# Kernel optimization log

Measured on AMD Instinct MI355X. Metric: run time of the kernel, lower is better.

Reference implementation:

```python
import jax, jax.numpy as jnp
import numpy as np
import math

B, C, T = 4, 512, 2048
LN_EPS = 1e-5

def setup_inputs() -> dict:
    key = jax.random.key(0)
    ks = jax.random.split(key, 12)
    s = 1.0 / math.sqrt(C)
    inp = {
        'feat': jax.random.normal(ks[0], (B, C, T), dtype=jnp.float32),
        'Wq': jax.random.normal(ks[1], (C, C), dtype=jnp.float32) * s,
        'bq': jax.random.normal(ks[2], (C,), dtype=jnp.float32) * s,
        'Wk': jax.random.normal(ks[3], (C, C), dtype=jnp.float32) * s,
        'bk': jax.random.normal(ks[4], (C,), dtype=jnp.float32) * s,
        'Wv': jax.random.normal(ks[5], (C, C), dtype=jnp.float32) * s,
        'bv': jax.random.normal(ks[6], (C,), dtype=jnp.float32) * s,
        'Ws': jax.random.normal(ks[7], (C, C), dtype=jnp.float32) * s,
        'bs': jax.random.normal(ks[8], (C,), dtype=jnp.float32) * s,
        'Wl': jax.random.normal(ks[9], (C,), dtype=jnp.float32) * s,
        'bl': jax.random.normal(ks[10], (1,), dtype=jnp.float32) * s,
    }
    return inp

def reference(feat, Wq, bq, Wk, bk, Wv, bv, Ws, bs, Wl, bl):
    d = feat.shape[1]
    # 1x1 Conv1d == per-position linear over channels. feat: [B,C,T]
    value = jnp.einsum('oc,bct->bto', Wv, feat) + bv          # [B,T,C]
    query = jnp.einsum('oc,bct->bto', Wq, feat) + bq          # [B,T,C]
    key_  = jnp.einsum('oc,bct->bct', Wk, feat) + bk[:, None] # [B,C,T]
    f = jnp.einsum('btc,bcs->bts', query, key_) / math.sqrt(d)
    f = jax.nn.softmax(f, axis=2)                             # [B,T,T]
    y = jnp.einsum('bts,bsc->btc', f, value)                  # [B,T,C]
    f_score = jax.nn.sigmoid(jnp.einsum('btc,c->bt', y, Wl) + bl[0])
    z = jnp.einsum('bts,bsc->btc', 1.0 - f, value)            # [B,T,C]
    b_score = 1.0 - jax.nn.sigmoid(jnp.einsum('btc,c->bt', z, Wl) + bl[0])
    f_score = (f_score + b_score) / 2.0
    y_ct = jnp.einsum('oc,btc->bot', Ws, y) + bs[:, None]     # smooth conv, [B,C,T]
    out = feat + y_ct
    # LayerNorm over (C, T) jointly, default affine (weight=1, bias=0)
    mu = jnp.mean(out, axis=(1, 2), keepdims=True)
    var = jnp.mean(jnp.square(out - mu), axis=(1, 2), keepdims=True)
    out = (out - mu) * jax.lax.rsqrt(var + LN_EPS)
    return out, f_score
```

## Files before the change

kernel.cpp:

```cpp
#include <hip/hip_runtime.h>
#include <hip/hip_bf16.h>

#define BB 4
#define CC 512
#define TT 2048
static constexpr long CT  = (long)CC * TT;
static constexpr long TC  = (long)TT * CC;
static constexpr long TTT = (long)TT * TT;
static constexpr float SM_SCALE = 0.04419417382415922f;

typedef __bf16 bf16;
typedef __attribute__((ext_vector_type(8))) __bf16 bf16x8;
typedef __attribute__((ext_vector_type(4))) __bf16 bf16x4;
typedef __attribute__((ext_vector_type(4))) float f32x4;

__device__ __forceinline__ void load_lds16(const bf16* g, bf16* l)
{
    __builtin_amdgcn_global_load_lds(
        (const __attribute__((address_space(1))) void*)g,
        (__attribute__((address_space(3))) void*)l, 16, 0, 0);
}

#define FENCE asm volatile("" ::: "memory")

template <int TM, int TN, int WR, int WC, int BK>
struct CorePipe {
    static constexpr int THREADS = WR * WC * 64;
    static constexpr int MI = TM / (WR * 16);
    static constexpr int NI = TN / (WC * 16);
    static constexpr int CPR = BK / 8;
    static constexpr int RSH = (BK == 64) ? 3 : 2;
    static constexpr int CMASK = CPR - 1;
    static constexpr int CHUNKS = (TM + TN) * CPR;
    static constexpr int ACH = TM * CPR;
    static constexpr int CPT = CHUNKS / THREADS;
    static_assert(CPT * THREADS == CHUNKS, "chunk divisibility");
    static_assert(CPT == 4, "vmcnt literals below assume 4 loads/thread/tile");

    __device__ static __forceinline__ void stage(
        const bf16* __restrict__ Ab, const bf16* __restrict__ Bb,
        int K, int m0, int n0, int t, int p, bf16* As, bf16* Bs, int tid)
    {
#pragma unroll
        for (int i = 0; i < CPT; ++i) {
            int c = tid + i * THREADS;
            if (c < ACH) {
                int row = c >> RSH;
                int gc  = (c & CMASK) ^ (row & CMASK);
                load_lds16(Ab + (long)(m0 + row) * K + t * BK + gc * 8,
                           As + p * (TM * BK) + c * 8);
            } else {
                int d = c - ACH;
                int row = d >> RSH;
                int gc  = (d & CMASK) ^ (row & CMASK);
                load_lds16(Bb + (long)(n0 + row) * K + t * BK + gc * 8,
                           Bs + p * (TN * BK) + d * 8);
            }
        }
    }

    __device__ static __forceinline__ void run(
        const bf16* __restrict__ Ab, const bf16* __restrict__ Bb,
        int K, int m0, int n0, bf16* As, bf16* Bs, f32x4 (&acc)[MI][NI])
    {
        const int tid  = threadIdx.x;
        const int lane = tid & 63;
        const int wid  = tid >> 6;
        const int wr = (wid / WC) * (MI * 16);
        const int wc = (wid % WC) * (NI * 16);
        const int lm = lane & 15;
        const int lq = lane >> 4;
        const int nt = K / BK;

        stage(Ab, Bb, K, m0, n0, 0, 0, As, Bs, tid);
        stage(Ab, Bb, K, m0, n0, 1, 1, As, Bs, tid);
        asm volatile("s_waitcnt vmcnt(4)" ::: "memory");
        FENCE; __builtin_amdgcn_s_barrier(); FENCE;

        for (int t = 0; t < nt; ++t) {
            const int p = t & 1;
            const bf16* Ap = As + p * (TM * BK);
            const bf16* Bp = Bs + p * (TN * BK);
            bf16x8 af[BK / 32][MI], bfr[BK / 32][NI];
#pragma unroll
            for (int ks = 0; ks < BK / 32; ++ks) {
#pragma unroll
                for (int i = 0; i < MI; ++i) {
                    int ar = wr + i * 16 + lm;
                    int cc = (ks * 4 + lq) ^ (ar & CMASK);
                    af[ks][i] = *(const bf16x8*)(Ap + ar * BK + cc * 8);
                }
#pragma unroll
                for (int i = 0; i < NI; ++i) {
                    int br = wc + i * 16 + lm;
                    int cc = (ks * 4 + lq) ^ (br & CMASK);
                    bfr[ks][i] = *(const bf16x8*)(Bp + br * BK + cc * 8);
                }
            }
            asm volatile("s_waitcnt lgkmcnt(0)" ::: "memory");
            __builtin_amdgcn_sched_barrier(0);
            FENCE; __builtin_amdgcn_s_barrier(); FENCE;
            if (t + 2 < nt)
                stage(Ab, Bb, K, m0, n0, t + 2, p, As, Bs, tid);
            __builtin_amdgcn_s_setprio(1);
#pragma unroll
            for (int ks = 0; ks < BK / 32; ++ks)
#pragma unroll
                for (int mi = 0; mi < MI; ++mi)
#pragma unroll
                    for (int ni = 0; ni < NI; ++ni)
                        acc[mi][ni] = __builtin_amdgcn_mfma_f32_16x16x32_bf16(
                            af[ks][mi], bfr[ks][ni], acc[mi][ni], 0, 0, 0);
            __builtin_amdgcn_s_setprio(0);
            if (t + 1 < nt) {
                if (t + 2 < nt)
                    asm volatile("s_waitcnt vmcnt(4)" ::: "memory");
                else
                    asm volatile("s_waitcnt vmcnt(0)" ::: "memory");
                FENCE; __builtin_amdgcn_s_barrier(); FENCE;
            }
        }
    }
};

using CP = CorePipe<128, 128, 4, 2, 64>;

struct CoreQVPipe {
    static constexpr int THREADS = 512;
    static constexpr int MI = 2;
    static constexpr int NI = 4;
    static constexpr int BK = 64;
    static constexpr int CPR = 8, RSH = 3, CMASK = 7;
    static constexpr int ACH = 128 * 8;
    static constexpr int CHUNKS = 256 * 8;
    static constexpr int CPT = CHUNKS / THREADS;

    __device__ static __forceinline__ void stage(
        const bf16* __restrict__ Ab, const bf16* __restrict__ Bq,
        const bf16* __restrict__ Bv, int m0, int t, int p,
        bf16* As, bf16* Bs, int tid)
    {
#pragma unroll
        for (int i = 0; i < CPT; ++i) {
            int c = tid + i * THREADS;
            if (c < ACH) {
                int row = c >> RSH;
                int gc  = (c & CMASK) ^ (row & CMASK);
                load_lds16(Ab + (long)(m0 + row) * 512 + t * 64 + gc * 8,
                           As + p * (128 * 64) + c * 8);
            } else {
                int d = c - ACH;
                int row = d >> RSH;
                int gc  = (d & CMASK) ^ (row & CMASK);
                const bf16* src = (row < 64)
                    ? Bq + (long)row * 512
                    : Bv + (long)(row - 64) * 512;
                load_lds16(src + t * 64 + gc * 8, Bs + p * (128 * 64) + d * 8);
            }
        }
    }

    __device__ static __forceinline__ void run(
        const bf16* __restrict__ Ab, const bf16* __restrict__ Bq,
        const bf16* __restrict__ Bv,
        int m0, bf16* As, bf16* Bs, f32x4 (&acc)[MI][NI])
    {
        const int tid  = threadIdx.x;
        const int lane = tid & 63;
        const int wid  = tid >> 6;
        const int wr = (wid / 2) * 32;
        const int wc = (wid % 2) * 64;
        const int lm = lane & 15;
        const int lq = lane >> 4;
        const int nt = 8;

        stage(Ab, Bq, Bv, m0, 0, 0, As, Bs, tid);
        stage(Ab, Bq, Bv, m0, 1, 1, As, Bs, tid);
        asm volatile("s_waitcnt vmcnt(4)" ::: "memory");
        FENCE; __builtin_amdgcn_s_barrier(); FENCE;

        for (int t = 0; t < nt; ++t) {
            const int p = t & 1;
            const bf16* Ap = As + p * (128 * 64);
            const bf16* Bp = Bs + p * (128 * 64);
            bf16x8 af[2][MI], bfr[2][NI];
#pragma unroll
            for (int ks = 0; ks < 2; ++ks) {
#pragma unroll
                for (int i = 0; i < MI; ++i) {
                    int ar = wr + i * 16 + lm;
                    int cc = (ks * 4 + lq) ^ (ar & CMASK);
                    af[ks][i] = *(const bf16x8*)(Ap + ar * BK + cc * 8);
                }
#pragma unroll
                for (int i = 0; i < NI; ++i) {
                    int br = wc + i * 16 + lm;
                    int cc = (ks * 4 + lq) ^ (br & CMASK);
                    bfr[ks][i] = *(const bf16x8*)(Bp + br * BK + cc * 8);
                }
            }
            asm volatile("s_waitcnt lgkmcnt(0)" ::: "memory");
            __builtin_amdgcn_sched_barrier(0);
            FENCE; __builtin_amdgcn_s_barrier(); FENCE;
            if (t + 2 < nt)
                stage(Ab, Bq, Bv, m0, t + 2, p, As, Bs, tid);
            __builtin_amdgcn_s_setprio(1);
#pragma unroll
            for (int ks = 0; ks < 2; ++ks)
#pragma unroll
                for (int mi = 0; mi < MI; ++mi)
#pragma unroll
                    for (int ni = 0; ni < NI; ++ni)
                        acc[mi][ni] = __builtin_amdgcn_mfma_f32_16x16x32_bf16(
                            af[ks][mi], bfr[ks][ni], acc[mi][ni], 0, 0, 0);
            __builtin_amdgcn_s_setprio(0);
            if (t + 1 < nt) {
                if (t + 2 < nt)
                    asm volatile("s_waitcnt vmcnt(4)" ::: "memory");
                else
                    asm volatile("s_waitcnt vmcnt(0)" ::: "memory");
                FENCE; __builtin_amdgcn_s_barrier(); FENCE;
            }
        }
    }
};

__global__ __launch_bounds__(512)
void gemm_qv_kernel(const bf16* __restrict__ featT, const bf16* __restrict__ Wq_bf,
                    const bf16* __restrict__ Wv_bf, bf16* __restrict__ Qb,
                    bf16* __restrict__ Vn, const float* __restrict__ bq,
                    const float* __restrict__ bv, const float* __restrict__ wkc,
                    const float* __restrict__ bk, float* __restrict__ qb,
                    const float* __restrict__ Wl, float* __restrict__ vl)
{
    __shared__ __align__(16) bf16 As[2 * 128 * 64];
    __shared__ __align__(16) bf16 Bs[2 * 128 * 64];
    const int rb = blockIdx.z;
    const int m0 = blockIdx.y * 128;
    const int ng = blockIdx.x;
    const long wofs = (long)(ng * 64) * 512;
    f32x4 acc[2][4] = {};
    CoreQVPipe::run(featT + (long)rb * TC, Wq_bf + wofs, Wv_bf + wofs, m0, As, Bs, acc);

    const int lane = threadIdx.x & 63, wid = threadIdx.x >> 6;
    const int wr = (wid / 2) * 32;
    const bool isV = wid & 1;
    const int lm = lane & 15, lq = lane >> 4;

    if (isV) {
        bf16* outV = Vn + (long)rb * TC;
        float* vlb = vl + (long)rb * TT;
        float vs_[2][4] = {};
#pragma unroll
        for (int mi = 0; mi < 2; ++mi)
#pragma unroll
            for (int ni = 0; ni < 4; ++ni) {
                int n = ng * 64 + ni * 16 + lm;
                float bn = bv[n], wn = Wl[n];
#pragma unroll
                for (int r = 0; r < 4; ++r) {
                    int m = m0 + wr + mi * 16 + lq * 4 + r;
                    float v = acc[mi][ni][r] + bn;
                    outV[(long)m * 512 + n] = (bf16)v;
                    vs_[mi][r] += v * wn;
                }
            }
#pragma unroll
        for (int mi = 0; mi < 2; ++mi)
#pragma unroll
            for (int r = 0; r < 4; ++r) {
                float s = vs_[mi][r];
                s += __shfl_xor(s, 1, 64); s += __shfl_xor(s, 2, 64);
                s += __shfl_xor(s, 4, 64); s += __shfl_xor(s, 8, 64);
                if (lm == 0)
                    atomicAdd(vlb + m0 + wr + mi * 16 + lq * 4 + r, s);
            }
    } else {
        bf16* out = Qb + (long)rb * TC;
        float* qbb = qb + (long)rb * TT;
        float rs[2][4] = {};
#pragma unroll
        for (int mi = 0; mi < 2; ++mi)
#pragma unroll
            for (int ni = 0; ni < 4; ++ni) {
                int n = ng * 64 + ni * 16 + lm;
                float bn = bq[n], wn = wkc[n], kn = bk[n];
#pragma unroll
                for (int r = 0; r < 4; ++r) {
                    int m = m0 + wr + mi * 16 + lq * 4 + r;
                    float v = acc[mi][ni][r] + bn;
                    rs[mi][r] += v * kn;
                    out[(long)m * 512 + n] = (bf16)(v * wn);
                }
            }
#pragma unroll
        for (int mi = 0; mi < 2; ++mi)
#pragma unroll
            for (int r = 0; r < 4; ++r) {
                float s = rs[mi][r];
                s += __shfl_xor(s, 1, 64); s += __shfl_xor(s, 2, 64);
                s += __shfl_xor(s, 4, 64); s += __shfl_xor(s, 8, 64);
                if (lm == 0)
                    atomicAdd(qbb + m0 + wr + mi * 16 + lq * 4 + r, s);
            }
    }
}

__global__ __launch_bounds__(512, 2)
void gemm_s256_kernel(const bf16* __restrict__ Qb, const bf16* __restrict__ featT,
                      bf16* __restrict__ S, const float* __restrict__ qb,
                      float* __restrict__ rsum, const float* __restrict__ vl,
                      float* __restrict__ u)
{
    __shared__ __align__(16) bf16 lds[2][2][256 * 64];
    const int id   = blockIdx.x;
    const int xcd  = id & 7, sIdx = id >> 3;
    const int bz   = xcd >> 1;
    const int n0   = (sIdx & 7) * 256;
    const int m0   = (((xcd & 1) << 2) + (sIdx >> 3)) * 256;
    const bf16* __restrict__ Ab = Qb + (long)bz * TC;
    const bf16* __restrict__ Bb = featT + (long)bz * TC;

    const int tid  = threadIdx.x;
    const int lane = tid & 63;
    const int wid  = tid >> 6;
    const int lm = lane & 15, lq = lane >> 4;
    const int wrb = (wid >> 2) * 64;
    const int wcb = (wid & 3) * 32;

    f32x4 acc[8][4] = {};

#define STAGE_HT(t, op, h)                                                    \
    do {                                                                      \
        const bf16* gp_ = (op) ? Bb : Ab;                                     \
        const int  br_  = ((op) ? n0 : m0) + (h) * 128;                       \
        bf16* lp_ = &lds[(t) & 1][op][(h) * 128 * 64];                        \
        _Pragma("unroll")                                                     \
        for (int i_ = 0; i_ < 2; ++i_) {                                      \
            int c_ = tid + i_ * 512;                                          \
            int r_ = c_ >> 3;                                                 \
            int g_ = (c_ & 7) ^ (r_ & 7);                                     \
            load_lds16(gp_ + (long)(br_ + r_) * 512 + (t) * 64 + g_ * 8,      \
                       lp_ + c_ * 8);                                         \
        }                                                                     \
    } while (0)

#define PHASE(t, qm, qn, doSt, st, sop, sh, doVm)                             \
    do {                                                                      \
        bf16x8 af[2][4], bfr[2][2];                                           \
        const bf16* Al_ = lds[(t) & 1][0];                                    \
        const bf16* Bl_ = lds[(t) & 1][1];                                    \
        _Pragma("unroll")                                                     \
        for (int ks = 0; ks < 2; ++ks) {                                      \
            _Pragma("unroll")                                                 \
            for (int j = 0; j < 4; ++j) {                                     \
                int ar = (qm) * 128 + wrb + j * 16 + lm;                      \
                int cc = (ks * 4 + lq) ^ (ar & 7);                            \
                af[ks][j] = *(const bf16x8*)(Al_ + ar * 64 + cc * 8);         \
            }                                                                 \
            _Pragma("unroll")                                                 \
            for (int j = 0; j < 2; ++j) {                                     \
                int br = (qn) * 128 + wcb + j * 16 + lm;                      \
                int cc = (ks * 4 + lq) ^ (br & 7);                            \
                bfr[ks][j] = *(const bf16x8*)(Bl_ + br * 64 + cc * 8);        \
            }                                                                 \
        }                                                                     \
        if (doSt) STAGE_HT(st, sop, sh);                                      \
        if (doVm) {                                                           \
            if ((t) < 6) asm volatile("s_waitcnt vmcnt(4)" ::: "memory");     \
            else         asm volatile("s_waitcnt vmcnt(0)" ::: "memory");     \
        }                                                                     \
        FENCE; __builtin_amdgcn_s_barrier(); FENCE;                           \
        __builtin_amdgcn_s_setprio(1);                                        \
        _Pragma("unroll")                                                     \
        for (int ks = 0; ks < 2; ++ks)                                        \
            _Pragma("unroll")                                                 \
            for (int j = 0; j < 4; ++j)                                       \
                _Pragma("unroll")                                             \
                for (int j2 = 0; j2 < 2; ++j2)                                \
                    acc[(qm) * 4 + j][(qn) * 2 + j2] =                        \
                        __builtin_amdgcn_mfma_f32_16x16x32_bf16(              \
                            af[ks][j], bfr[ks][j2],                           \
                            acc[(qm) * 4 + j][(qn) * 2 + j2], 0, 0, 0);       \
        __builtin_amdgcn_s_setprio(0);                                        \
        FENCE; __builtin_amdgcn_s_barrier(); FENCE;                           \
    } while (0)

    STAGE_HT(0, 0, 0); STAGE_HT(0, 1, 0); STAGE_HT(0, 0, 1); STAGE_HT(0, 1, 1);
    STAGE_HT(1, 0, 0); STAGE_HT(1, 1, 0);
    asm volatile("s_waitcnt vmcnt(4)" ::: "memory");
    FENCE; __builtin_amdgcn_s_barrier(); FENCE;

    for (int t = 0; t < 8; ++t) {
        PHASE(t, 0, 0, t + 1 < 8, t + 1, 0, 1, false);
        PHASE(t, 0, 1, t + 1 < 8, t + 1, 1, 1, false);
        PHASE(t, 1, 0, t + 2 < 8, t + 2, 0, 0, false);
        PHASE(t, 1, 1, t + 2 < 8, t + 2, 1, 0, true);
    }
#undef PHASE
#undef STAGE_HT

    bf16* outp = S + (long)bz * TTT;
    const float* qbb = qb + (long)bz * TT;
    const float* vlb = vl + (long)bz * TT;
    float* rsb = rsum + (long)bz * TT;
    float* ub  = u + (long)bz * TT;
#pragma unroll
    for (int mi = 0; mi < 8; ++mi) {
        const int mrow = m0 + (mi >> 2) * 128 + wrb + (mi & 3) * 16 + lq * 4;
        const f32x4 qv = *(const f32x4*)(qbb + mrow);
        float rp[4] = {0.f, 0.f, 0.f, 0.f};
        float up[4] = {0.f, 0.f, 0.f, 0.f};
#pragma unroll
        for (int ni = 0; ni < 4; ++ni) {
            const int ncol = n0 + (ni >> 1) * 128 + wcb + (ni & 1) * 16 + lm;
            const float vlv = vlb[ncol];
#pragma unroll
            for (int r = 0; r < 4; ++r) {
                float p = __expf((acc[mi][ni][r] + qv[r]) * SM_SCALE);
                outp[(long)(mrow + r) * 2048 + ncol] = (bf16)p;
                rp[r] += p;
                up[r] += p * vlv;
            }
        }
#pragma unroll
        for (int r = 0; r < 4; ++r) {
            float s2 = rp[r], s3 = up[r];
            s2 += __shfl_xor(s2, 1, 64); s2 += __shfl_xor(s2, 2, 64);
            s2 += __shfl_xor(s2, 4, 64); s2 += __shfl_xor(s2, 8, 64);
            s3 += __shfl_xor(s3, 1, 64); s3 += __shfl_xor(s3, 2, 64);
            s3 += __shfl_xor(s3, 4, 64); s3 += __shfl_xor(s3, 8, 64);
            if (lm == 0) {
                atomicAdd(rsb + mrow + r, s2);
                atomicAdd(ub + mrow + r, s3);
            }
        }
    }
}

__global__ __launch_bounds__(512)
void gemm_vs_kernel(const bf16* __restrict__ Vn, const bf16* __restrict__ Ws_bf,
                    bf16* __restrict__ Vpt)
{
    __shared__ __align__(16) bf16 As[2 * 128 * 64];
    __shared__ __align__(16) bf16 Bs[2 * 128 * 64];
    const int id = blockIdx.x;
    const int xcd = id & 7, s = id >> 3;
    const int bz = xcd >> 1;
    const int m0 = (((xcd & 1) << 1) + (s >> 4)) * 128;
    const int n0 = (s & 15) * 128;
    f32x4 acc[2][4] = {};
    CP::run(Ws_bf, Vn + (long)bz * TC, 512, m0, n0, As, Bs, acc);

    const int lane = threadIdx.x & 63, wid = threadIdx.x >> 6;
    const int wr = (wid / 2) * 32, wc = (wid % 2) * 64;
    const int lm = lane & 15, lq = lane >> 4;
    bf16* out = Vpt + (long)bz * CT;
#pragma unroll
    for (int mi = 0; mi < 2; ++mi)
#pragma unroll
        for (int ni = 0; ni < 4; ++ni) {
            int n = n0 + wc + ni * 16 + lm;
#pragma unroll
            for (int r = 0; r < 4; ++r) {
                int m = m0 + wr + mi * 16 + lq * 4 + r;
                out[(long)m * 2048 + n] = (bf16)acc[mi][ni][r];
            }
        }
}

__global__ __launch_bounds__(512)
void gemm_out_kernel(const bf16* __restrict__ S, const bf16* __restrict__ Vpt,
                     float* __restrict__ out, const float* __restrict__ bs,
                     const float* __restrict__ feat,
                     const float* __restrict__ rsum, double* __restrict__ stats)
{
    __shared__ __align__(16) bf16 As[2 * 128 * 64];
    __shared__ __align__(16) bf16 Bs[2 * 128 * 64];
    __shared__ float red[16];
    const int id = blockIdx.x;
    const int xcd = id & 7, s = id >> 3;
    const int bz = xcd >> 1;
    const int n0 = (s & 3) * 128;
    const int m0 = (((xcd & 1) << 3) + (s >> 2)) * 128;
    f32x4 acc[2][4] = {};
    CP::run(S + (long)bz * TTT, Vpt + (long)bz * CT, 2048, m0, n0, As, Bs, acc);

    const int tid = threadIdx.x;
    const int lane = tid & 63, wid = tid >> 6;
    const int wr = (wid / 2) * 32, wc = (wid % 2) * 64;
    const int lm = lane & 15, lq = lane >> 4;
    const float* rsb = rsum + (long)bz * TT;
    float inv[2][4];
#pragma unroll
    for (int mi = 0; mi < 2; ++mi) {
        int mrow = m0 + wr + mi * 16 + lq * 4;
        f32x4 rv = *(const f32x4*)(rsb + mrow);
#pragma unroll
        for (int r = 0; r < 4; ++r) inv[mi][r] = 1.f / rv[r];
    }
    float s1 = 0.f, s2 = 0.f;
#pragma unroll
    for (int mi = 0; mi < 2; ++mi)
#pragma unroll
        for (int ni = 0; ni < 4; ++ni) {
            int mrow = m0 + wr + mi * 16 + lq * 4;
            int n = n0 + wc + ni * 16 + lm;
            long off = (long)bz * CT + (long)n * TT + mrow;
            f32x4 fv = *(const f32x4*)(feat + off);
            float bn = bs[n];
            f32x4 res;
#pragma unroll
            for (int r = 0; r < 4; ++r) {
                float v = acc[mi][ni][r] * inv[mi][r] + bn + fv[r];
                res[r] = v;
                s1 += v;
                s2 += v * v;
            }
            *(f32x4*)(out + off) = res;
        }
#pragma unroll
    for (int off = 32; off; off >>= 1) {
        s1 += __shfl_xor(s1, off, 64);
        s2 += __shfl_xor(s2, off, 64);
    }
    if (lane == 0) { red[wid] = s1; red[8 + wid] = s2; }
    __syncthreads();
    if (tid == 0) {
        double t1 = 0.0, t2 = 0.0;
#pragma unroll
        for (int w = 0; w < 8; ++w) { t1 += red[w]; t2 += red[8 + w]; }
        atomicAdd(stats + bz * 2, t1);
        atomicAdd(stats + bz * 2 + 1, t2);
    }
}

__global__ __launch_bounds__(256)
void prep_kernel(const float* __restrict__ feat, bf16* __restrict__ featT,
                 const float* __restrict__ Wq, const float* __restrict__ Wv,
                 const float* __restrict__ Ws, bf16* __restrict__ Wbf,
                 const float* __restrict__ Wk, const float* __restrict__ Wl,
                 const float* __restrict__ bv, float* __restrict__ wkc,
                 float* __restrict__ wvl, float* __restrict__ wlbv,
                 float* __restrict__ frp, float* __restrict__ qb,
                 float* __restrict__ u, float* __restrict__ rsum,
                 double* __restrict__ stats, float* __restrict__ vl)
{
    const int blk = blockIdx.x;
    const int tid = threadIdx.x;
    if (blk < 4096) {
        __shared__ float tile[32][33];
        __shared__ float sfr[4][32];
        const int b  = blk >> 10;
        const int c0 = ((blk & 1023) >> 6) * 32;
        const int tt = blk & 63;
        const int t0 = tt * 32;
        const int tx = tid & 31;
        const int ty = tid >> 5;
#pragma unroll
        for (int j = 0; j < 4; ++j) {
            int c = c0 + ty + j * 8;
            tile[ty + j * 8][tx] = feat[(long)b * CT + (long)c * TT + t0 + tx];
        }
        __syncthreads();
        float ps = 0.f;
#pragma unroll
        for (int j = 0; j < 4; ++j) {
            int tl = ty + j * 8;
            int t = t0 + tl;
            int c = c0 + tx;
            float v = tile[tx][tl];
            ps += v;
            featT[(long)b * TC + (long)t * CC + c] = (bf16)v;
        }
        const int wid = tid >> 6;
        ps += __shfl_xor(ps, 32, 64);
        if ((tid & 63) < 32) sfr[wid][tx] = ps;
        __syncthreads();
        if (tid < 32) {
            float s = sfr[0][tid] + sfr[1][tid] + sfr[2][tid] + sfr[3][tid];
            frp[(((long)b * 64 + tt) << 9) + c0 + tid] = s;
        }
    } else if (blk < 4480) {
        long gid = (long)(blk - 4096) * 256 + tid;
        long idx = gid * 8;
        int w = (int)(idx >> 18);
        long off = idx & 262143;
        const float* src = (w == 0) ? Wq : (w == 1) ? Wv : Ws;
        f32x4 a = *(const f32x4*)(src + off);
        f32x4 b = *(const f32x4*)(src + off + 4);
        bf16x8 o;
#pragma unroll
        for (int j = 0; j < 4; ++j) { o[j] = (bf16)a[j]; o[4 + j] = (bf16)b[j]; }
        *(bf16x8*)(Wbf + idx) = o;
    } else {
        int mid = (blk - 4480) * 256 + tid;
        if (mid < 512) {
            float s = 0.f;
            for (int o = 0; o < 512; ++o) s += Wk[o * 512 + mid];
            wkc[mid] = s;
        } else if (mid < 1024) {
            int k = mid - 512;
            float s = 0.f;
            for (int c = 0; c < 512; ++c) s += Wl[c] * Wv[c * 512 + k];
            wvl[k] = s;
        } else if (mid < 1088) {
            int lane = mid - 1024;
            float s = 0.f;
#pragma unroll
            for (int j = 0; j < 8; ++j) s += Wl[lane + 64 * j] * bv[lane + 64 * j];
#pragma unroll
            for (int off = 32; off; off >>= 1) s += __shfl_xor(s, off, 64);
            if (lane == 0) wlbv[0] = s;
        } else if (mid >= 1152 && mid < 1160) {
            stats[mid - 1152] = 0.0;
        } else if (mid >= 4096 && mid < 12288) {
            qb[mid - 4096] = 0.f;
        } else if (mid >= 12288 && mid < 20480) {
            u[mid - 12288] = 0.f;
        } else if (mid >= 20480 && mid < 28672) {
            rsum[mid - 20480] = 0.f;
        } else if (mid >= 28672 && mid < 36864) {
            vl[mid - 28672] = 0.f;
        }
    }
}

__global__ __launch_bounds__(256)
void ln_score_kernel(float* __restrict__ out, const double* __restrict__ stats,
                     const float* __restrict__ u, const float* __restrict__ frp,
                     const float* __restrict__ wvl, const float* __restrict__ wlbv,
                     const float* __restrict__ blp, const float* __restrict__ rsum)
{
    if (blockIdx.x < 4096) {
        long i = ((long)blockIdx.x * 256 + threadIdx.x) * 4;
        int b = (int)(i >> 20);
        const double n = 1048576.0;
        double mu  = stats[b * 2] / n;
        double var = stats[b * 2 + 1] / n - mu * mu;
        float rs = (float)(1.0 / sqrt(var + 1e-5));
        float muf = (float)mu;
        f32x4 v = *(f32x4*)(out + i);
#pragma unroll
        for (int j = 0; j < 4; ++j) v[j] = (v[j] - muf) * rs;
        *(f32x4*)(out + i) = v;
    } else {
        const int b = blockIdx.x - 4096;
        __shared__ float ssv[4];
        const int tid = threadIdx.x, lane = tid & 63, wid = tid >> 6;
        const float* fb = frp + ((long)b * 64 << 9);
        float s0 = 0.f, s1 = 0.f;
#pragma unroll 8
        for (int k = 0; k < 64; ++k) {
            s0 += fb[(k << 9) + tid];
            s1 += fb[(k << 9) + tid + 256];
        }
        float p = s0 * wvl[tid] + s1 * wvl[tid + 256];
#pragma unroll
        for (int off = 32; off; off >>= 1) p += __shfl_xor(p, off, 64);
        if (lane == 0) ssv[wid] = p;
        __syncthreads();
        const float sv = ssv[0] + ssv[1] + ssv[2] + ssv[3] + 2048.f * wlbv[0];
        const float bl0 = blp[0];
#pragma unroll
        for (int j = 0; j < 8; ++j) {
            int t = tid + j * 256;
            float uu = u[(long)b * TT + t] / rsum[(long)b * TT + t];
            float uf = uu + bl0;
            float vf = sv - uu + bl0;
            float fs  = 1.f / (1.f + __expf(-uf));
            float bsc = 1.f - 1.f / (1.f + __expf(-vf));
            out[(long)BB * CT + (long)b * TT + t] = 0.5f * (fs + bsc);
        }
    }
}

extern "C" void kernel_launch(void* const* d_in, const int* in_sizes, int n_in,
                              void* d_out, int out_size, void* d_ws, size_t ws_size,
                              hipStream_t stream)
{
    const float* feat = (const float*)d_in[0];
    const float* Wq   = (const float*)d_in[1];
    const float* bq   = (const float*)d_in[2];
    const float* Wk   = (const float*)d_in[3];
    const float* bk   = (const float*)d_in[4];
    const float* Wv   = (const float*)d_in[5];
    const float* bv   = (const float*)d_in[6];
    const float* Ws   = (const float*)d_in[7];
    const float* bs   = (const float*)d_in[8];
    const float* Wl   = (const float*)d_in[9];
    const float* bl   = (const float*)d_in[10];
    float* out = (float*)d_out;

    if (ws_size < 69316736) return;
    char* ws = (char*)d_ws;
    bf16* featT  = (bf16*)(ws);
    bf16* Wbf    = (bf16*)(ws + 8388608);
    bf16* Qb     = (bf16*)(ws + 9961472);
    bf16* Vn     = (bf16*)(ws + 18350080);
    bf16* Vpt    = (bf16*)(ws + 26738688);
    float* vl    = (float*)(ws + 26738688);
    bf16* S      = (bf16*)(ws + 35127296);
    float* wkc   = (float*)(ws + 68689920);
    float* wvl   = (float*)(ws + 68691968);
    float* wlbv  = (float*)(ws + 68694016);
    float* qb    = (float*)(ws + 68694080);
    double* stats= (double*)(ws + 68726848);
    float* u     = (float*)(ws + 68726912);
    float* rsum  = (float*)(ws + 68759680);
    float* frp   = (float*)(ws + 68792448);

    bf16* Wq_bf = Wbf;
    bf16* Wv_bf = Wbf + 262144;
    bf16* Ws_bf = Wbf + 524288;

    prep_kernel<<<4624, 256, 0, stream>>>(feat, featT, Wq, Wv, Ws, Wbf, Wk, Wl, bv,
                                          wkc, wvl, wlbv, frp, qb, u, rsum, stats, vl);
    gemm_qv_kernel<<<dim3(8, 16, 4), 512, 0, stream>>>(
        featT, Wq_bf, Wv_bf, Qb, Vn, bq, bv, wkc, bk, qb, Wl, vl);
    gemm_s256_kernel<<<256, 512, 0, stream>>>(Qb, featT, S, qb, rsum, vl, u);
    gemm_vs_kernel<<<256, 512, 0, stream>>>(Vn, Ws_bf, Vpt);
    gemm_out_kernel<<<256, 512, 0, stream>>>(S, Vpt, out, bs, feat, rsum, stats);
    ln_score_kernel<<<4100, 256, 0, stream>>>(out, stats, u, frp, wvl, wlbv, bl, rsum);
}
```

Before: 211.7 us.

## Fuse score GEMM, softmax and PV GEMM into a single flash-style kernel

Replaces the separate S=QK^T kernel, which wrote a full bf16 TxT probability matrix per batch, and the following S·V GEMM with one fused kernel. Each block holds 32 query rows, computes 64-wide score tiles, exponentiates them into LDS, and accumulates P·V on chip, with row sums and u computed locally instead of through atomics. This removes the large S write and re-read plus the rsum/u zeroing. The cost is a small 32-row tile with only 256 blocks, and each block re-streams all K and V tiles, so lower parallelism and more redundant loads may offset the saved traffic.

Measured after the change: 260.6 us. 23.1% more time.

```diff
diff --git a/kernel.cpp b/kernel.cpp
--- a/kernel.cpp
+++ b/kernel.cpp
@@ -6,7 +6,6 @@
 #define TT 2048
 static constexpr long CT  = (long)CC * TT;
 static constexpr long TC  = (long)TT * CC;
-static constexpr long TTT = (long)TT * TT;
 static constexpr float SM_SCALE = 0.04419417382415922f;
 
 typedef __bf16 bf16;
@@ -23,19 +22,27 @@
 
 #define FENCE asm volatile("" ::: "memory")
 
+template <int N> __device__ __forceinline__ void vm_wait()
+{
+    if constexpr (N == 0)      asm volatile("s_waitcnt vmcnt(0)" ::: "memory");
+    else if constexpr (N == 1) asm volatile("s_waitcnt vmcnt(1)" ::: "memory");
+    else if constexpr (N == 2) asm volatile("s_waitcnt vmcnt(2)" ::: "memory");
+    else if constexpr (N == 4) asm volatile("s_waitcnt vmcnt(4)" ::: "memory");
+    else static_assert(N == 0, "unsupported vmcnt literal");
+}
+
 template <int TM, int TN, int WR, int WC, int BK>
 struct CorePipe {
     static constexpr int THREADS = WR * WC * 64;
     static constexpr int MI = TM / (WR * 16);
     static constexpr int NI = TN / (WC * 16);
     static constexpr int CPR = BK / 8;
-    static constexpr int RSH = (BK == 64) ? 3 : 2;
+    static constexpr int RSH = 3;
     static constexpr int CMASK = CPR - 1;
     static constexpr int CHUNKS = (TM + TN) * CPR;
     static constexpr int ACH = TM * CPR;
     static constexpr int CPT = CHUNKS / THREADS;
     static_assert(CPT * THREADS == CHUNKS, "chunk divisibility");
-    static_assert(CPT == 4, "vmcnt literals below assume 4 loads/thread/tile");
 
     __device__ static __forceinline__ void stage(
         const bf16* __restrict__ Ab, const bf16* __restrict__ Bb,
@@ -74,7 +81,7 @@
 
         stage(Ab, Bb, K, m0, n0, 0, 0, As, Bs, tid);
         stage(Ab, Bb, K, m0, n0, 1, 1, As, Bs, tid);
-        asm volatile("s_waitcnt vmcnt(4)" ::: "memory");
+        vm_wait<4>();
         FENCE; __builtin_amdgcn_s_barrier(); FENCE;
 
         for (int t = 0; t < nt; ++t) {
@@ -113,27 +120,18 @@
                             af[ks][mi], bfr[ks][ni], acc[mi][ni], 0, 0, 0);
             __builtin_amdgcn_s_setprio(0);
             if (t + 1 < nt) {
-                if (t + 2 < nt)
-                    asm volatile("s_waitcnt vmcnt(4)" ::: "memory");
-                else
-                    asm volatile("s_waitcnt vmcnt(0)" ::: "memory");
+                if (t + 2 < nt) vm_wait<4>();
+                else            vm_wait<0>();
                 FENCE; __builtin_amdgcn_s_barrier(); FENCE;
             }
         }
     }
 };
 
-using CP = CorePipe<128, 128, 4, 2, 64>;
+using CPVS = CorePipe<128, 128, 4, 2, 64>;
 
 struct CoreQVPipe {
-    static constexpr int THREADS = 512;
-    static constexpr int MI = 2;
-    static constexpr int NI = 4;
-    static constexpr int BK = 64;
-    static constexpr int CPR = 8, RSH = 3, CMASK = 7;
     static constexpr int ACH = 128 * 8;
-    static constexpr int CHUNKS = 256 * 8;
-    static constexpr int CPT = CHUNKS / THREADS;
 
     __device__ static __forceinline__ void stage(
         const bf16* __restrict__ Ab, const bf16* __restrict__ Bq,
@@ -141,17 +139,17 @@
         bf16* As, bf16* Bs, int tid)
     {
 #pragma unroll
-        for (int i = 0; i < CPT; ++i) {
-            int c = tid + i * THREADS;
+        for (int i = 0; i < 4; ++i) {
+            int c = tid + i * 512;
             if (c < ACH) {
-                int row = c >> RSH;
-                int gc  = (c & CMASK) ^ (row & CMASK);
+                int row = c >> 3;
+                int gc  = (c & 7) ^ (row & 7);
                 load_lds16(Ab + (long)(m0 + row) * 512 + t * 64 + gc * 8,
                            As + p * (128 * 64) + c * 8);
             } else {
                 int d = c - ACH;
-                int row = d >> RSH;
-                int gc  = (d & CMASK) ^ (row & CMASK);
+                int row = d >> 3;
+                int gc  = (d & 7) ^ (row & 7);
                 const bf16* src = (row < 64)
                     ? Bq + (long)row * 512
                     : Bv + (long)(row - 64) * 512;
@@ -163,7 +161,7 @@
     __device__ static __forceinline__ void run(
         const bf16* __restrict__ Ab, const bf16* __restrict__ Bq,
         const bf16* __restrict__ Bv,
-        int m0, bf16* As, bf16* Bs, f32x4 (&acc)[MI][NI])
+        int m0, bf16* As, bf16* Bs, f32x4 (&acc)[2][4])
     {
         const int tid  = threadIdx.x;
         const int lane = tid & 63;
@@ -176,27 +174,27 @@
 
         stage(Ab, Bq, Bv, m0, 0, 0, As, Bs, tid);
         stage(Ab, Bq, Bv, m0, 1, 1, As, Bs, tid);
-        asm volatile("s_waitcnt vmcnt(4)" ::: "memory");
+        vm_wait<4>();
         FENCE; __builtin_amdgcn_s_barrier(); FENCE;
 
         for (int t = 0; t < nt; ++t) {
             const int p = t & 1;
             const bf16* Ap = As + p * (128 * 64);
             const bf16* Bp = Bs + p * (128 * 64);
-            bf16x8 af[2][MI], bfr[2][NI];
+            bf16x8 af[2][2], bfr[2][4];
 #pragma unroll
             for (int ks = 0; ks < 2; ++ks) {
 #pragma unroll
-                for (int i = 0; i < MI; ++i) {
+                for (int i = 0; i < 2; ++i) {
                     int ar = wr + i * 16 + lm;
-                    int cc = (ks * 4 + lq) ^ (ar & CMASK);
-                    af[ks][i] = *(const bf16x8*)(Ap + ar * BK + cc * 8);
+                    int cc = (ks * 4 + lq) ^ (ar & 7);
+                    af[ks][i] = *(const bf16x8*)(Ap + ar * 64 + cc * 8);
                 }
 #pragma unroll
-                for (int i = 0; i < NI; ++i) {
+                for (int i = 0; i < 4; ++i) {
                     int br = wc + i * 16 + lm;
-                    int cc = (ks * 4 + lq) ^ (br & CMASK);
-                    bfr[ks][i] = *(const bf16x8*)(Bp + br * BK + cc * 8);
+                    int cc = (ks * 4 + lq) ^ (br & 7);
+                    bfr[ks][i] = *(const bf16x8*)(Bp + br * 64 + cc * 8);
                 }
             }
             asm volatile("s_waitcnt lgkmcnt(0)" ::: "memory");
@@ -208,17 +206,15 @@
 #pragma unroll
             for (int ks = 0; ks < 2; ++ks)
 #pragma unroll
-                for (int mi = 0; mi < MI; ++mi)
-#pragma unroll
-                    for (int ni = 0; ni < NI; ++ni)
+                for (int mi = 0; mi < 2; ++mi)
+#pragma unroll
+                    for (int ni = 0; ni < 4; ++ni)
                         acc[mi][ni] = __builtin_amdgcn_mfma_f32_16x16x32_bf16(
                             af[ks][mi], bfr[ks][ni], acc[mi][ni], 0, 0, 0);
             __builtin_amdgcn_s_setprio(0);
             if (t + 1 < nt) {
-                if (t + 2 < nt)
-                    asm volatile("s_waitcnt vmcnt(4)" ::: "memory");
-                else
-                    asm volatile("s_waitcnt vmcnt(0)" ::: "memory");
+                if (t + 2 < nt) vm_wait<4>();
+                else            vm_wait<0>();
                 FENCE; __builtin_amdgcn_s_barrier(); FENCE;
             }
         }
@@ -306,138 +302,6 @@
     }
 }
 
-__global__ __launch_bounds__(512, 2)
-void gemm_s256_kernel(const bf16* __restrict__ Qb, const bf16* __restrict__ featT,
-                      bf16* __restrict__ S, const float* __restrict__ qb,
-                      float* __restrict__ rsum, const float* __restrict__ vl,
-                      float* __restrict__ u)
-{
-    __shared__ __align__(16) bf16 lds[2][2][256 * 64];
-    const int id   = blockIdx.x;
-    const int xcd  = id & 7, sIdx = id >> 3;
-    const int bz   = xcd >> 1;
-    const int n0   = (sIdx & 7) * 256;
-    const int m0   = (((xcd & 1) << 2) + (sIdx >> 3)) * 256;
-    const bf16* __restrict__ Ab = Qb + (long)bz * TC;
-    const bf16* __restrict__ Bb = featT + (long)bz * TC;
-
-    const int tid  = threadIdx.x;
-    const int lane = tid & 63;
-    const int wid  = tid >> 6;
-    const int lm = lane & 15, lq = lane >> 4;
-    const int wrb = (wid >> 2) * 64;
-    const int wcb = (wid & 3) * 32;
-
-    f32x4 acc[8][4] = {};
-
-#define STAGE_HT(t, op, h)                                                    \
-    do {                                                                      \
-        const bf16* gp_ = (op) ? Bb : Ab;                                     \
-        const int  br_  = ((op) ? n0 : m0) + (h) * 128;                       \
-        bf16* lp_ = &lds[(t) & 1][op][(h) * 128 * 64];                        \
-        _Pragma("unroll")                                                     \
-        for (int i_ = 0; i_ < 2; ++i_) {                                      \
-            int c_ = tid + i_ * 512;                                          \
-            int r_ = c_ >> 3;                                                 \
-            int g_ = (c_ & 7) ^ (r_ & 7);                                     \
-            load_lds16(gp_ + (long)(br_ + r_) * 512 + (t) * 64 + g_ * 8,      \
-                       lp_ + c_ * 8);                                         \
-        }                                                                     \
-    } while (0)
-
-#define PHASE(t, qm, qn, doSt, st, sop, sh, doVm)                             \
-    do {                                                                      \
-        bf16x8 af[2][4], bfr[2][2];                                           \
-        const bf16* Al_ = lds[(t) & 1][0];                                    \
-        const bf16* Bl_ = lds[(t) & 1][1];                                    \
-        _Pragma("unroll")                                                     \
-        for (int ks = 0; ks < 2; ++ks) {                                      \
-            _Pragma("unroll")                                                 \
-            for (int j = 0; j < 4; ++j) {                                     \
-                int ar = (qm) * 128 + wrb + j * 16 + lm;                      \
-                int cc = (ks * 4 + lq) ^ (ar & 7);                            \
-                af[ks][j] = *(const bf16x8*)(Al_ + ar * 64 + cc * 8);         \
-            }                                                                 \
-            _Pragma("unroll")                                                 \
-            for (int j = 0; j < 2; ++j) {                                     \
-                int br = (qn) * 128 + wcb + j * 16 + lm;                      \
-                int cc = (ks * 4 + lq) ^ (br & 7);                            \
-                bfr[ks][j] = *(const bf16x8*)(Bl_ + br * 64 + cc * 8);        \
-            }                                                                 \
-        }                                                                     \
-        if (doSt) STAGE_HT(st, sop, sh);                                      \
-        if (doVm) {                                                           \
-            if ((t) < 6) asm volatile("s_waitcnt vmcnt(4)" ::: "memory");     \
-            else         asm volatile("s_waitcnt vmcnt(0)" ::: "memory");     \
-        }                                                                     \
-        FENCE; __builtin_amdgcn_s_barrier(); FENCE;                           \
-        __builtin_amdgcn_s_setprio(1);                                        \
-        _Pragma("unroll")                                                     \
-        for (int ks = 0; ks < 2; ++ks)                                        \
-            _Pragma("unroll")                                                 \
-            for (int j = 0; j < 4; ++j)                                       \
-                _Pragma("unroll")                                             \
-                for (int j2 = 0; j2 < 2; ++j2)                                \
-                    acc[(qm) * 4 + j][(qn) * 2 + j2] =                        \
-                        __builtin_amdgcn_mfma_f32_16x16x32_bf16(              \
-                            af[ks][j], bfr[ks][j2],                           \
-                            acc[(qm) * 4 + j][(qn) * 2 + j2], 0, 0, 0);       \
-        __builtin_amdgcn_s_setprio(0);                                        \
-        FENCE; __builtin_amdgcn_s_barrier(); FENCE;                           \
-    } while (0)
-
-    STAGE_HT(0, 0, 0); STAGE_HT(0, 1, 0); STAGE_HT(0, 0, 1); STAGE_HT(0, 1, 1);
-    STAGE_HT(1, 0, 0); STAGE_HT(1, 1, 0);
-    asm volatile("s_waitcnt vmcnt(4)" ::: "memory");
-    FENCE; __builtin_amdgcn_s_barrier(); FENCE;
-
-    for (int t = 0; t < 8; ++t) {
-        PHASE(t, 0, 0, t + 1 < 8, t + 1, 0, 1, false);
-        PHASE(t, 0, 1, t + 1 < 8, t + 1, 1, 1, false);
-        PHASE(t, 1, 0, t + 2 < 8, t + 2, 0, 0, false);
-        PHASE(t, 1, 1, t + 2 < 8, t + 2, 1, 0, true);
-    }
-#undef PHASE
-#undef STAGE_HT
-
-    bf16* outp = S + (long)bz * TTT;
-    const float* qbb = qb + (long)bz * TT;
-    const float* vlb = vl + (long)bz * TT;
-    float* rsb = rsum + (long)bz * TT;
-    float* ub  = u + (long)bz * TT;
-#pragma unroll
-    for (int mi = 0; mi < 8; ++mi) {
-        const int mrow = m0 + (mi >> 2) * 128 + wrb + (mi & 3) * 16 + lq * 4;
-        const f32x4 qv = *(const f32x4*)(qbb + mrow);
-        float rp[4] = {0.f, 0.f, 0.f, 0.f};
-        float up[4] = {0.f, 0.f, 0.f, 0.f};
-#pragma unroll
-        for (int ni = 0; ni < 4; ++ni) {
-            const int ncol = n0 + (ni >> 1) * 128 + wcb + (ni & 1) * 16 + lm;
-            const float vlv = vlb[ncol];
-#pragma unroll
-            for (int r = 0; r < 4; ++r) {
-                float p = __expf((acc[mi][ni][r] + qv[r]) * SM_SCALE);
-                outp[(long)(mrow + r) * 2048 + ncol] = (bf16)p;
-                rp[r] += p;
-                up[r] += p * vlv;
-            }
-        }
-#pragma unroll
-        for (int r = 0; r < 4; ++r) {
-            float s2 = rp[r], s3 = up[r];
-            s2 += __shfl_xor(s2, 1, 64); s2 += __shfl_xor(s2, 2, 64);
-            s2 += __shfl_xor(s2, 4, 64); s2 += __shfl_xor(s2, 8, 64);
-            s3 += __shfl_xor(s3, 1, 64); s3 += __shfl_xor(s3, 2, 64);
-            s3 += __shfl_xor(s3, 4, 64); s3 += __shfl_xor(s3, 8, 64);
-            if (lm == 0) {
-                atomicAdd(rsb + mrow + r, s2);
-                atomicAdd(ub + mrow + r, s3);
-            }
-        }
-    }
-}
-
 __global__ __launch_bounds__(512)
 void gemm_vs_kernel(const bf16* __restrict__ Vn, const bf16* __restrict__ Ws_bf,
                     bf16* __restrict__ Vpt)
@@ -450,7 +314,7 @@
     const int m0 = (((xcd & 1) << 1) + (s >> 4)) * 128;
     const int n0 = (s & 15) * 128;
     f32x4 acc[2][4] = {};
-    CP::run(Ws_bf, Vn + (long)bz * TC, 512, m0, n0, As, Bs, acc);
+    CPVS::run(Ws_bf, Vn + (long)bz * TC, 512, m0, n0, As, Bs, acc);
 
     const int lane = threadIdx.x & 63, wid = threadIdx.x >> 6;
     const int wr = (wid / 2) * 32, wc = (wid % 2) * 64;
@@ -470,49 +334,198 @@
 }
 
 __global__ __launch_bounds__(512)
-void gemm_out_kernel(const bf16* __restrict__ S, const bf16* __restrict__ Vpt,
-                     float* __restrict__ out, const float* __restrict__ bs,
-                     const float* __restrict__ feat,
-                     const float* __restrict__ rsum, double* __restrict__ stats)
+void flash_kernel(const bf16* __restrict__ Qb, const bf16* __restrict__ featT,
+                  const bf16* __restrict__ Vpt, const float* __restrict__ qb,
+                  const float* __restrict__ vl, float* __restrict__ u,
+                  float* __restrict__ out, const float* __restrict__ bs,
+                  const float* __restrict__ feat, double* __restrict__ stats)
 {
-    __shared__ __align__(16) bf16 As[2 * 128 * 64];
-    __shared__ __align__(16) bf16 Bs[2 * 128 * 64];
+    __shared__ __align__(16) bf16 Qs[8 * 32 * 64];
+    __shared__ __align__(16) bf16 Ks[3 * 64 * 64];
+    __shared__ __align__(16) bf16 Ps[32 * 64];
+    __shared__ __align__(16) bf16 Vs[512 * 64];
+    __shared__ float srs[4][32];
+    __shared__ float sus[4][32];
     __shared__ float red[16];
+
     const int id = blockIdx.x;
-    const int xcd = id & 7, s = id >> 3;
+    const int xcd = id & 7, sIdx = id >> 3;
     const int bz = xcd >> 1;
-    const int n0 = (s & 3) * 128;
-    const int m0 = (((xcd & 1) << 3) + (s >> 2)) * 128;
-    f32x4 acc[2][4] = {};
-    CP::run(S + (long)bz * TTT, Vpt + (long)bz * CT, 2048, m0, n0, As, Bs, acc);
+    const int m0 = (((xcd & 1) << 5) + sIdx) * 32;
 
     const int tid = threadIdx.x;
     const int lane = tid & 63, wid = tid >> 6;
-    const int wr = (wid / 2) * 32, wc = (wid % 2) * 64;
     const int lm = lane & 15, lq = lane >> 4;
-    const float* rsb = rsum + (long)bz * TT;
+    const int wrS = wid >> 2, wcS = wid & 3;
+
+    const bf16* Qg = Qb + (long)bz * TC;
+    const bf16* Kg = featT + (long)bz * TC;
+    const bf16* Vg = Vpt + (long)bz * CT;
+
+#define STAGE_V(s0)                                                          \
+    do { _Pragma("unroll")                                                   \
+        for (int i_ = 0; i_ < 8; ++i_) {                                     \
+            int c_ = tid + i_ * 512;                                         \
+            int r_ = c_ >> 3, ch_ = c_ & 7;                                  \
+            int g_ = ch_ ^ (r_ & 7);                                         \
+            load_lds16(Vg + (long)r_ * 2048 + (s0) + g_ * 8, Vs + c_ * 8);   \
+        } } while (0)
+#define STAGE_K(s0, kb, sl)                                                  \
+    do {                                                                     \
+        int r_ = tid >> 3, ch_ = tid & 7;                                    \
+        int g_ = ch_ ^ (r_ & 7);                                             \
+        load_lds16(Kg + (long)((s0) + r_) * 512 + (kb) * 64 + g_ * 8,        \
+                   Ks + (sl) * 4096 + tid * 8);                              \
+    } while (0)
+
+#pragma unroll
+    for (int i = 0; i < 4; ++i) {
+        int c = tid + i * 512;
+        int kb = c >> 8, r_ = (c >> 3) & 31, ch = c & 7;
+        int gc = ch ^ (r_ & 7);
+        load_lds16(Qg + (long)(m0 + r_) * 512 + kb * 64 + gc * 8, Qs + c * 8);
+    }
+    STAGE_V(0);
+    STAGE_K(0, 0, 0); STAGE_K(0, 1, 1); STAGE_K(0, 2, 2);
+
+    const f32x4 qv4 = *(const f32x4*)(qb + (long)bz * TT + m0 + wrS * 16 + lq * 4);
+    const float* vlb = vl + (long)bz * TT;
+
+    f32x4 oacc[2][4] = {};
+    float rs_acc[4] = {0.f, 0.f, 0.f, 0.f};
+    float u_acc[4]  = {0.f, 0.f, 0.f, 0.f};
+
+    for (int t = 0; t < 32; ++t) {
+        const int s0 = t * 64;
+        vm_wait<2>();
+        FENCE; __builtin_amdgcn_s_barrier(); FENCE;
+
+        f32x4 sacc = {0.f, 0.f, 0.f, 0.f};
+#pragma unroll
+        for (int kb = 0; kb < 8; ++kb) {
+            const int sl = kb % 3;
+            bf16x8 aq[2], bk_[2];
+#pragma unroll
+            for (int ks = 0; ks < 2; ++ks) {
+                int ar = wrS * 16 + lm;
+                int cc = (ks * 4 + lq) ^ (ar & 7);
+                aq[ks] = *(const bf16x8*)(Qs + ((kb * 32 + ar) * 8 + cc) * 8);
+                int br = wcS * 16 + lm;
+                int c2 = (ks * 4 + lq) ^ (br & 7);
+                bk_[ks] = *(const bf16x8*)(Ks + sl * 4096 + (br * 8 + c2) * 8);
+            }
+            asm volatile("s_waitcnt lgkmcnt(0)" ::: "memory");
+            __builtin_amdgcn_sched_barrier(0);
+            FENCE; __builtin_amdgcn_s_barrier(); FENCE;
+            if (kb + 3 < 8) STAGE_K(s0, kb + 3, sl);
+            __builtin_amdgcn_s_setprio(1);
+#pragma unroll
+            for (int ks = 0; ks < 2; ++ks)
+                sacc = __builtin_amdgcn_mfma_f32_16x16x32_bf16(
+                    aq[ks], bk_[ks], sacc, 0, 0, 0);
+            __builtin_amdgcn_s_setprio(0);
+            if (kb < 7) {
+                if (kb < 5)       vm_wait<2>();
+                else if (kb == 5) vm_wait<1>();
+                else              vm_wait<0>();
+                FENCE; __builtin_amdgcn_s_barrier(); FENCE;
+            }
+        }
+
+        const float vlv = vlb[s0 + wcS * 16 + lm];
+        const int prow0 = wrS * 16 + lq * 4;
+        const int pcol  = wcS * 16 + lm;
+#pragma unroll
+        for (int r = 0; r < 4; ++r) {
+            float p = __expf((sacc[r] + qv4[r]) * SM_SCALE);
+            rs_acc[r] += p;
+            u_acc[r]  += p * vlv;
+            int row = prow0 + r;
+            int swch = (pcol >> 3) ^ (row & 7);
+            Ps[row * 64 + swch * 8 + (pcol & 7)] = (bf16)p;
+        }
+        asm volatile("s_waitcnt lgkmcnt(0)" ::: "memory");
+        FENCE; __builtin_amdgcn_s_barrier(); FENCE;
+
+        bf16x8 pa[2][2], vb[2][4];
+#pragma unroll
+        for (int ks = 0; ks < 2; ++ks) {
+#pragma unroll
+            for (int mi = 0; mi < 2; ++mi) {
+                int ar = mi * 16 + lm;
+                int cc = (ks * 4 + lq) ^ (ar & 7);
+                pa[ks][mi] = *(const bf16x8*)(Ps + ar * 64 + cc * 8);
+            }
+#pragma unroll
+            for (int ni = 0; ni < 4; ++ni) {
+                int br = wid * 64 + ni * 16 + lm;
+                int cc = (ks * 4 + lq) ^ (br & 7);
+                vb[ks][ni] = *(const bf16x8*)(Vs + br * 64 + cc * 8);
+            }
+        }
+        asm volatile("s_waitcnt lgkmcnt(0)" ::: "memory");
+        __builtin_amdgcn_sched_barrier(0);
+        FENCE; __builtin_amdgcn_s_barrier(); FENCE;
+        if (t + 1 < 32) {
+            STAGE_V(s0 + 64);
+            STAGE_K(s0 + 64, 0, 0); STAGE_K(s0 + 64, 1, 1); STAGE_K(s0 + 64, 2, 2);
+        }
+        __builtin_amdgcn_s_setprio(1);
+#pragma unroll
+        for (int ks = 0; ks < 2; ++ks)
+#pragma unroll
+            for (int mi = 0; mi < 2; ++mi)
+#pragma unroll
+                for (int ni = 0; ni < 4; ++ni)
+                    oacc[mi][ni] = __builtin_amdgcn_mfma_f32_16x16x32_bf16(
+                        pa[ks][mi], vb[ks][ni], oacc[mi][ni], 0, 0, 0);
+        __builtin_amdgcn_s_setprio(0);
+    }
+#undef STAGE_V
+#undef STAGE_K
+
+#pragma unroll
+    for (int r = 0; r < 4; ++r) {
+        float a = rs_acc[r], b = u_acc[r];
+        a += __shfl_xor(a, 1, 64); a += __shfl_xor(a, 2, 64);
+        a += __shfl_xor(a, 4, 64); a += __shfl_xor(a, 8, 64);
+        b += __shfl_xor(b, 1, 64); b += __shfl_xor(b, 2, 64);
+        b += __shfl_xor(b, 4, 64); b += __shfl_xor(b, 8, 64);
+        if (lm == 0) {
+            srs[wcS][wrS * 16 + lq * 4 + r] = a;
+            sus[wcS][wrS * 16 + lq * 4 + r] = b;
+        }
+    }
+    asm volatile("s_waitcnt lgkmcnt(0)" ::: "memory");
+    FENCE; __builtin_amdgcn_s_barrier(); FENCE;
+    if (tid < 32) {
+        float rt = srs[0][tid] + srs[1][tid] + srs[2][tid] + srs[3][tid];
+        float ut = sus[0][tid] + sus[1][tid] + sus[2][tid] + sus[3][tid];
+        u[(long)bz * TT + m0 + tid] = ut / rt;
+    }
     float inv[2][4];
 #pragma unroll
-    for (int mi = 0; mi < 2; ++mi) {
-        int mrow = m0 + wr + mi * 16 + lq * 4;
-        f32x4 rv = *(const f32x4*)(rsb + mrow);
-#pragma unroll
-        for (int r = 0; r < 4; ++r) inv[mi][r] = 1.f / rv[r];
-    }
+    for (int mi = 0; mi < 2; ++mi)
+#pragma unroll
+        for (int r = 0; r < 4; ++r) {
+            int row = mi * 16 + lq * 4 + r;
+            inv[mi][r] = 1.f /
+                (srs[0][row] + srs[1][row] + srs[2][row] + srs[3][row]);
+        }
     float s1 = 0.f, s2 = 0.f;
 #pragma unroll
     for (int mi = 0; mi < 2; ++mi)
 #pragma unroll
         for (int ni = 0; ni < 4; ++ni) {
-            int mrow = m0 + wr + mi * 16 + lq * 4;
-            int n = n0 + wc + ni * 16 + lm;
+            int mrow = m0 + mi * 16 + lq * 4;
+            int n = wid * 64 + ni * 16 + lm;
             long off = (long)bz * CT + (long)n * TT + mrow;
             f32x4 fv = *(const f32x4*)(feat + off);
             float bn = bs[n];
             f32x4 res;
 #pragma unroll
             for (int r = 0; r < 4; ++r) {
-                float v = acc[mi][ni][r] * inv[mi][r] + bn + fv[r];
+                float v = oacc[mi][ni][r] * inv[mi][r] + bn + fv[r];
                 res[r] = v;
                 s1 += v;
                 s2 += v * v;
@@ -543,7 +556,6 @@
                  const float* __restrict__ bv, float* __restrict__ wkc,
                  float* __restrict__ wvl, float* __restrict__ wlbv,
                  float* __restrict__ frp, float* __restrict__ qb,
-                 float* __restrict__ u, float* __restrict__ rsum,
                  double* __restrict__ stats, float* __restrict__ vl)
 {
     const int blk = blockIdx.x;
@@ -616,10 +628,6 @@
             stats[mid - 1152] = 0.0;
         } else if (mid >= 4096 && mid < 12288) {
             qb[mid - 4096] = 0.f;
-        } else if (mid >= 12288 && mid < 20480) {
-            u[mid - 12288] = 0.f;
-        } else if (mid >= 20480 && mid < 28672) {
-            rsum[mid - 20480] = 0.f;
         } else if (mid >= 28672 && mid < 36864) {
             vl[mid - 28672] = 0.f;
         }
@@ -630,7 +638,7 @@
 void ln_score_kernel(float* __restrict__ out, const double* __restrict__ stats,
                      const float* __restrict__ u, const float* __restrict__ frp,
                      const float* __restrict__ wvl, const float* __restrict__ wlbv,
-                     const float* __restrict__ blp, const float* __restrict__ rsum)
+                     const float* __restrict__ blp)
 {
     if (blockIdx.x < 4096) {
         long i = ((long)blockIdx.x * 256 + threadIdx.x) * 4;
@@ -665,7 +673,7 @@
 #pragma unroll
         for (int j = 0; j < 8; ++j) {
             int t = tid + j * 256;
-            float uu = u[(long)b * TT + t] / rsum[(long)b * TT + t];
+            float uu = u[(long)b * TT + t];
             float uf = uu + bl0;
             float vf = sv - uu + bl0;
             float fs  = 1.f / (1.f + __expf(-uf));
@@ -692,34 +700,32 @@
     const float* bl   = (const float*)d_in[10];
     float* out = (float*)d_out;
 
-    if (ws_size < 69316736) return;
+    if (ws_size < 69349504) return;
     char* ws = (char*)d_ws;
     bf16* featT  = (bf16*)(ws);
     bf16* Wbf    = (bf16*)(ws + 8388608);
     bf16* Qb     = (bf16*)(ws + 9961472);
     bf16* Vn     = (bf16*)(ws + 18350080);
     bf16* Vpt    = (bf16*)(ws + 26738688);
-    float* vl    = (float*)(ws + 26738688);
-    bf16* S      = (bf16*)(ws + 35127296);
     float* wkc   = (float*)(ws + 68689920);
     float* wvl   = (float*)(ws + 68691968);
     float* wlbv  = (float*)(ws + 68694016);
     float* qb    = (float*)(ws + 68694080);
     double* stats= (double*)(ws + 68726848);
     float* u     = (float*)(ws + 68726912);
-    float* rsum  = (float*)(ws + 68759680);
     float* frp   = (float*)(ws + 68792448);
+    float* vl    = (float*)(ws + 69316736);
 
     bf16* Wq_bf = Wbf;
     bf16* Wv_bf = Wbf + 262144;
     bf16* Ws_bf = Wbf + 524288;
 
     prep_kernel<<<4624, 256, 0, stream>>>(feat, featT, Wq, Wv, Ws, Wbf, Wk, Wl, bv,
-                                          wkc, wvl, wlbv, frp, qb, u, rsum, stats, vl);
+                                          wkc, wvl, wlbv, frp, qb, stats, vl);
     gemm_qv_kernel<<<dim3(8, 16, 4), 512, 0, stream>>>(
         featT, Wq_bf, Wv_bf, Qb, Vn, bq, bv, wkc, bk, qb, Wl, vl);
-    gemm_s256_kernel<<<256, 512, 0, stream>>>(Qb, featT, S, qb, rsum, vl, u);
     gemm_vs_kernel<<<256, 512, 0, stream>>>(Vn, Ws_bf, Vpt);
-    gemm_out_kernel<<<256, 512, 0, stream>>>(S, Vpt, out, bs, feat, rsum, stats);
-    ln_score_kernel<<<4100, 256, 0, stream>>>(out, stats, u, frp, wvl, wlbv, bl, rsum);
+    flash_kernel<<<256, 512, 0, stream>>>(Qb, featT, Vpt, qb, vl, u,
+                                          out, bs, feat, stats);
+    ln_score_kernel<<<4100, 256, 0, stream>>>(out, stats, u, frp, wvl, wlbv, bl);
 }
```
